# Kernel optimization log

Measured on AMD Instinct MI355X. Metric: run time of the kernel, lower is better.

The kernel has to match this reference:

```python
import jax, jax.numpy as jnp
import numpy as np

N, D_IN, D_HID, N_EXPERTS, TOP_K = 16384, 2048, 2048, 8, 2


def setup_inputs() -> dict:
    key = jax.random.key(0)
    k1, k2, k3, k4, k5 = jax.random.split(key, 5)
    x = jax.random.normal(k1, (N, D_IN), dtype=jnp.float32)
    W_experts = jax.random.normal(k2, (N_EXPERTS, D_IN, D_HID), dtype=jnp.float32) * 0.02
    b_experts = jax.random.normal(k3, (N_EXPERTS, D_HID), dtype=jnp.float32) * 0.02
    W_gate = jax.random.normal(k4, (D_IN, N_EXPERTS), dtype=jnp.float32) * 0.02
    b_gate = jax.random.normal(k5, (N_EXPERTS,), dtype=jnp.float32) * 0.02
    return {"x": x, "W_experts": W_experts, "b_experts": b_experts,
            "W_gate": W_gate, "b_gate": b_gate}


def reference(x, W_experts, b_experts, W_gate, b_gate):
    # gating softmax over experts: [N, E]
    gates = jax.nn.softmax(x @ W_gate + b_gate, axis=-1)
    # per-token top-k scores/indices: [N, K]
    top_scores, top_idx = jax.lax.top_k(gates, TOP_K)
    # FAITHFUL to original: experts chosen by the FIRST token's indices for all tokens
    idx0 = top_idx[0]                       # [K]
    W_sel = W_experts[idx0]                 # [K, D_IN, D_HID]
    b_sel = b_experts[idx0]                 # [K, D_HID]
    expert_out = jnp.einsum('ni,kio->nko', x, W_sel) + b_sel[None]  # [N, K, D_HID]
    # weight by each token's own top-k scores and sum over the K experts
    return (expert_out * top_scores[:, :, None]).sum(axis=1)        # [N, D_HID]
```

## Files before the change

kernel.cpp:

```cpp
#include <hip/hip_runtime.h>
#include <hip/hip_bf16.h>
#include <stdint.h>

#define N_TOK 16384
#define D_IN  2048
#define D_HID 2048

typedef __attribute__((ext_vector_type(8))) short  bf16x8;
typedef __attribute__((ext_vector_type(4))) float  f32x4;
typedef __attribute__((ext_vector_type(8))) unsigned short u16x8;

__device__ __forceinline__ unsigned short f2bf(float f) {
    unsigned int u = __float_as_uint(f);
    u = (u + 0x7FFFu + ((u >> 16) & 1u)) >> 16;
    return (unsigned short)u;
}

__global__ void gate_kernel(const float* __restrict__ x,
                            const float* __restrict__ Wg,
                            const float* __restrict__ bg,
                            float* __restrict__ s12,
                            int* __restrict__ eidx) {
    const int token = blockIdx.x * 4 + (threadIdx.x >> 6);
    const int lane  = threadIdx.x & 63;
    const float* xr = x + (size_t)token * D_IN;

    float acc[8];
#pragma unroll
    for (int e = 0; e < 8; ++e) acc[e] = 0.f;

    for (int i = lane; i < D_IN; i += 64) {
        float xv = xr[i];
        const float4* wr = (const float4*)(Wg + (size_t)i * 8);
        float4 w0 = wr[0], w1 = wr[1];
        acc[0] += xv * w0.x; acc[1] += xv * w0.y;
        acc[2] += xv * w0.z; acc[3] += xv * w0.w;
        acc[4] += xv * w1.x; acc[5] += xv * w1.y;
        acc[6] += xv * w1.z; acc[7] += xv * w1.w;
    }
#pragma unroll
    for (int off = 32; off > 0; off >>= 1) {
#pragma unroll
        for (int e = 0; e < 8; ++e) acc[e] += __shfl_xor(acc[e], off);
    }

    float lg[8];
    float mx = -1e30f;
#pragma unroll
    for (int e = 0; e < 8; ++e) { lg[e] = acc[e] + bg[e]; mx = fmaxf(mx, lg[e]); }
    float sum = 0.f;
#pragma unroll
    for (int e = 0; e < 8; ++e) { lg[e] = expf(lg[e] - mx); sum += lg[e]; }
    float inv = 1.f / sum;

    float s1 = -1.f, s2 = -1.f; int i1 = 0, i2 = 0;
#pragma unroll
    for (int e = 0; e < 8; ++e) {
        float g = lg[e] * inv;
        if (g > s1)      { s2 = s1; i2 = i1; s1 = g; i1 = e; }
        else if (g > s2) { s2 = g;  i2 = e; }
    }
    if (lane == 0) {
        s12[token * 2]     = s1;
        s12[token * 2 + 1] = s2;
        if (token == 0) { eidx[0] = i1; eidx[1] = i2; }
    }
}

__global__ __launch_bounds__(256) void xconv_kernel(
    const float* __restrict__ x, unsigned short* __restrict__ xb) {
    const int mt = blockIdx.x >> 6;
    const int kt = blockIdx.x & 63;
    const int t  = threadIdx.x;
    const float* src = x + ((size_t)(mt * 256 + t)) * D_IN + kt * 32;
    unsigned short* slab = xb + ((size_t)(mt * 64 + kt)) * 8192;
#pragma unroll
    for (int ks = 0; ks < 4; ++ks) {
        float4 a = *(const float4*)(src + ks * 8);
        float4 b = *(const float4*)(src + ks * 8 + 4);
        u16x8 v;
        v[0] = f2bf(a.x); v[1] = f2bf(a.y); v[2] = f2bf(a.z); v[3] = f2bf(a.w);
        v[4] = f2bf(b.x); v[5] = f2bf(b.y); v[6] = f2bf(b.z); v[7] = f2bf(b.w);
        *(u16x8*)(slab + (ks * 256 + t) * 8) = v;
    }
}

__global__ void wconv_kernel(const float* __restrict__ W,
                             const int* __restrict__ eidx,
                             unsigned short* __restrict__ wbT) {
    __shared__ float tile[64][65];
    const int be  = blockIdx.z;
    const int e   = eidx[be];
    const int k0  = blockIdx.y * 64;
    const int n0  = blockIdx.x * 64;
    const int bx  = n0 >> 7;
    const int cl0 = n0 & 127;
    const int kt0 = k0 >> 5;
    const float* src = W + (size_t)e * D_IN * D_HID;
    const int t = threadIdx.x;

#pragma unroll
    for (int p = 0; p < 4; ++p) {
        int row = p * 16 + (t >> 4);
        int col = (t & 15) * 4;
        const float* s = src + (size_t)(k0 + row) * D_HID + n0 + col;
        tile[row][col]     = s[0];
        tile[row][col + 1] = s[1];
        tile[row][col + 2] = s[2];
        tile[row][col + 3] = s[3];
    }
    __syncthreads();

    const int g   = (t >> 5) * 8;
    const int ktl = t >> 7;
    const int ks  = (t >> 5) & 3;
#pragma unroll
    for (int p = 0; p < 2; ++p) {
        int n = p * 32 + (t & 31);
        u16x8 v;
#pragma unroll
        for (int j = 0; j < 8; ++j) v[j] = f2bf(tile[g + j][n]);
        unsigned short* dst = wbT + ((size_t)(bx * 64 + kt0 + ktl)) * 8192 +
                              ((size_t)(ks * 256 + be * 128 + cl0 + n)) * 8;
        *(u16x8*)dst = v;
    }
}

#define GLD16(gp, lp)                                                        \
    __builtin_amdgcn_global_load_lds(                                        \
        (const __attribute__((address_space(1))) void*)(gp),                 \
        (__attribute__((address_space(3))) void*)(lp), 16, 0, 0)

#define LDSV(SLOT) (*(const bf16x8*)&lds[(SLOT) * 8])

#define PHASE(CB, P, T1, DOSTAGE, VMSTR)                                     \
    do {                                                                     \
        const int hb = (CB) * 4096 + ((P) >> 1) * 2048;                      \
        if (((P) & 1) == 0) {                                                \
            bC[0] = LDSV(hb + 1024 + bro);                                   \
            bC[1] = LDSV(hb + 1024 + bro + 16);                              \
            bC[2] = LDSV(hb + 1024 + bro + 32);                              \
            bC[3] = LDSV(hb + 1024 + bro + 48);                              \
        }                                                                    \
        aP[0] = LDSV(hb + aro + ((P) & 1) * 64);                             \
        aP[1] = LDSV(hb + aro + ((P) & 1) * 64 + 16);                        \
        aP[2] = LDSV(hb + aro + ((P) & 1) * 64 + 32);                        \
        aP[3] = LDSV(hb + aro + ((P) & 1) * 64 + 48);                        \
        if (DOSTAGE) {                                                       \
            const size_t so = ((size_t)(2 * (T1) + ((P) >> 1)) * 1024 +      \
                               ((P) & 1) * 512) * 8;                         \
            const int dd = ((CB) ^ 1) * 4096 + ((P) >> 1) * 2048 +           \
                           ((P) & 1) * 512 + t512;                           \
            GLD16(gA0 + so, &lds[dd * 8]);                                   \
            GLD16(gB0 + so, &lds[(dd + 1024) * 8]);                          \
        }                                                                    \
        if (VMSTR[0]) asm volatile(VMSTR ::: "memory");                      \
        __builtin_amdgcn_s_barrier();                                        \
        asm volatile("s_waitcnt lgkmcnt(0)" ::: "memory");                   \
        __builtin_amdgcn_sched_barrier(0);                                   \
        __builtin_amdgcn_s_setprio(1);                                       \
        _Pragma("unroll")                                                    \
        for (int mi = 0; mi < 4; ++mi)                                       \
            _Pragma("unroll")                                                \
            for (int ni = 0; ni < 4; ++ni)                                   \
                acc[((P) & 1) * 4 + mi][ni] =                                \
                    __builtin_amdgcn_mfma_f32_16x16x32_bf16(                 \
                        aP[mi], bC[ni], acc[((P) & 1) * 4 + mi][ni], 0, 0, 0); \
        __builtin_amdgcn_s_setprio(0);                                       \
        __builtin_amdgcn_s_barrier();                                        \
    } while (0)

__global__ __launch_bounds__(512, 2) void moe_gemm_kernel(
    const unsigned short* __restrict__ xb,
    const unsigned short* __restrict__ wbT,
    const float* __restrict__ b_exp,
    const int* __restrict__ eidx,
    const float* __restrict__ s12,
    float* __restrict__ out) {
    __shared__ __align__(16) short lds[2 * 4096 * 8];

    const int t512 = threadIdx.x;
    const int lane = t512 & 63;
    const int w    = t512 >> 6;
    const int wm   = w >> 2;
    const int wn   = w & 3;

    const int bid = blockIdx.x;
    const int xcd = bid & 7;
    const int jb  = bid >> 3;
    const int bx  = xcd * 2 + (jb & 1);
    const int by  = jb >> 1;
    const int mbase = by * 256;
    const int nbase = bx * 128;

    const unsigned short* gA0 = xb  + ((size_t)by * 64) * 8192 + t512 * 8;
    const unsigned short* gB0 = wbT + ((size_t)bx * 64) * 8192 + t512 * 8;

    const int aro = (lane >> 4) * 256 + wm * 128 + (lane & 15);
    const int bro = (lane >> 4) * 256 + wn * 64 + (lane & 15);

    f32x4 acc[8][4];
#pragma unroll
    for (int mi = 0; mi < 8; ++mi)
#pragma unroll
        for (int ni = 0; ni < 4; ++ni) acc[mi][ni] = (f32x4){0.f, 0.f, 0.f, 0.f};

    bf16x8 aP[4], bC[4];

#pragma unroll
    for (int p = 0; p < 4; ++p) {
        const size_t so = ((size_t)(p >> 1) * 1024 + (p & 1) * 512) * 8;
        const int dd = (p >> 1) * 2048 + (p & 1) * 512 + t512;
        GLD16(gA0 + so, &lds[dd * 8]);
        GLD16(gB0 + so, &lds[(dd + 1024) * 8]);
    }
    asm volatile("s_waitcnt vmcnt(4)" ::: "memory");
    __builtin_amdgcn_s_barrier();

    int cb = 0;
    for (int t = 0; t < 31; ++t) {
        PHASE(cb, 0, t + 1, 1, "");
        PHASE(cb, 1, t + 1, 1, "s_waitcnt vmcnt(4)");
        PHASE(cb, 2, t + 1, 1, "");
        PHASE(cb, 3, t + 1, 1, "s_waitcnt vmcnt(4)");
        cb ^= 1;
    }
    PHASE(1, 0, 0, 0, "");
    PHASE(1, 1, 0, 0, "s_waitcnt vmcnt(0)");
    PHASE(1, 2, 0, 0, "");
    PHASE(1, 3, 0, 0, "");

    __syncthreads();
    float* fl = (float*)lds;
    if (wn >= 2) {
        float* reg = fl + (wm * 2 + (wn - 2)) * 8192;
#pragma unroll
        for (int mi = 0; mi < 8; ++mi)
#pragma unroll
            for (int ni = 0; ni < 4; ++ni)
#pragma unroll
                for (int j = 0; j < 4; ++j) {
                    int row_l = mi * 16 + ((lane >> 4) << 2) + j;
                    int col_l = ni * 16 + (lane & 15);
                    reg[row_l * 64 + col_l] = acc[mi][ni][j];
                }
    }
    __syncthreads();
    if (wn < 2) {
        const float* reg = fl + (wm * 2 + wn) * 8192;
        const int e0 = eidx[0], e1 = eidx[1];
        const float* bb0 = b_exp + (size_t)e0 * D_HID;
        const float* bb1 = b_exp + (size_t)e1 * D_HID;
        const float2* s12v = (const float2*)s12;
        int   cc[4];
        float b0c[4], b1c[4];
#pragma unroll
        for (int ni = 0; ni < 4; ++ni) {
            cc[ni]  = nbase + wn * 64 + ni * 16 + (lane & 15);
            b0c[ni] = bb0[cc[ni]];
            b1c[ni] = bb1[cc[ni]];
        }
#pragma unroll
        for (int mi = 0; mi < 8; ++mi)
#pragma unroll
            for (int j = 0; j < 4; ++j) {
                int row_l = mi * 16 + ((lane >> 4) << 2) + j;
                int r = mbase + wm * 128 + row_l;
                float2 s = s12v[r];
#pragma unroll
                for (int ni = 0; ni < 4; ++ni) {
                    float y1 = reg[row_l * 64 + ni * 16 + (lane & 15)];
                    out[(size_t)r * D_HID + cc[ni]] =
                        s.x * (acc[mi][ni][j] + b0c[ni]) + s.y * (y1 + b1c[ni]);
                }
            }
    }
}

extern "C" void kernel_launch(void* const* d_in, const int* in_sizes, int n_in,
                              void* d_out, int out_size, void* d_ws, size_t ws_size,
                              hipStream_t stream) {
    const float* x         = (const float*)d_in[0];
    const float* W_experts = (const float*)d_in[1];
    const float* b_experts = (const float*)d_in[2];
    const float* W_gate    = (const float*)d_in[3];
    const float* b_gate    = (const float*)d_in[4];
    float* out = (float*)d_out;

    char* ws = (char*)d_ws;
    float* s12  = (float*)ws;
    int*   eidx = (int*)(ws + 131072);
    unsigned short* xb  = (unsigned short*)(ws + 262144);
    unsigned short* wbT = (unsigned short*)(ws + 262144 + 67108864);

    gate_kernel<<<N_TOK / 4, 256, 0, stream>>>(x, W_gate, b_gate, s12, eidx);
    xconv_kernel<<<4096, 256, 0, stream>>>(x, xb);
    wconv_kernel<<<dim3(32, 32, 2), 256, 0, stream>>>(W_experts, eidx, wbT);
    moe_gemm_kernel<<<1024, 512, 0, stream>>>(xb, wbT, b_experts, eidx, s12, out);
}
```

Measured before the change: 341.4 us.

## Rewrite GEMM with 32x32 MFMA, 4-stage pipeline, merge gate and x-convert kernels

The MoE GEMM now runs 256-thread blocks with 32x32x16 bf16 MFMA, so each wave computes a 128x128 sub-tile. It uses a 4-buffer LDS ring with three K tiles in flight instead of the previous double-buffered 16x16 phase scheme with barriers on both sides. The gating and x-to-bf16 conversion kernels are merged into one launch, and the gating path now handles 8 tokens per wave to reuse the W_gate loads. The intent is better MFMA density, fewer barriers and one fewer launch. In exchange the GEMM runs one block per CU with a much larger accumulator register footprint, and the new LDS addressing may create bank conflicts.

Measured after the change: 377.5 us. +10.6%, slower.

```diff
diff --git a/kernel.cpp b/kernel.cpp
--- a/kernel.cpp
+++ b/kernel.cpp
@@ -6,9 +6,9 @@
 #define D_IN  2048
 #define D_HID 2048
 
-typedef __attribute__((ext_vector_type(8))) short  bf16x8;
-typedef __attribute__((ext_vector_type(4))) float  f32x4;
-typedef __attribute__((ext_vector_type(8))) unsigned short u16x8;
+typedef __attribute__((ext_vector_type(8)))  short bf16x8;
+typedef __attribute__((ext_vector_type(16))) float f32x16;
+typedef __attribute__((ext_vector_type(8)))  unsigned short u16x8;
 
 __device__ __forceinline__ unsigned short f2bf(float f) {
     unsigned int u = __float_as_uint(f);
@@ -16,72 +16,88 @@
     return (unsigned short)u;
 }
 
-__global__ void gate_kernel(const float* __restrict__ x,
-                            const float* __restrict__ Wg,
-                            const float* __restrict__ bg,
-                            float* __restrict__ s12,
-                            int* __restrict__ eidx) {
-    const int token = blockIdx.x * 4 + (threadIdx.x >> 6);
-    const int lane  = threadIdx.x & 63;
-    const float* xr = x + (size_t)token * D_IN;
-
-    float acc[8];
-#pragma unroll
-    for (int e = 0; e < 8; ++e) acc[e] = 0.f;
+__global__ __launch_bounds__(256) void prep_kernel(
+    const float* __restrict__ x,
+    const float* __restrict__ Wg,
+    const float* __restrict__ bg,
+    unsigned short* __restrict__ xb,
+    float* __restrict__ s12,
+    int* __restrict__ eidx) {
+    const int bid = blockIdx.x;
+    if (bid < 4096) {
+        const int mt = bid >> 6;
+        const int kt = bid & 63;
+        const int t  = threadIdx.x;
+        const float* src = x + ((size_t)(mt * 256 + t)) * D_IN + kt * 32;
+        unsigned short* slab = xb + ((size_t)(mt * 64 + kt)) * 8192;
+#pragma unroll
+        for (int ks = 0; ks < 4; ++ks) {
+            float4 a = *(const float4*)(src + ks * 8);
+            float4 b = *(const float4*)(src + ks * 8 + 4);
+            u16x8 v;
+            v[0] = f2bf(a.x); v[1] = f2bf(a.y); v[2] = f2bf(a.z); v[3] = f2bf(a.w);
+            v[4] = f2bf(b.x); v[5] = f2bf(b.y); v[6] = f2bf(b.z); v[7] = f2bf(b.w);
+            *(u16x8*)(slab + (ks * 256 + t) * 8) = v;
+        }
+        return;
+    }
+    const int gb   = bid - 4096;
+    const int w    = threadIdx.x >> 6;
+    const int lane = threadIdx.x & 63;
+    const int tbase = gb * 32 + w * 8;
+
+    float acc[8][8];
+#pragma unroll
+    for (int tok = 0; tok < 8; ++tok)
+#pragma unroll
+        for (int e = 0; e < 8; ++e) acc[tok][e] = 0.f;
 
     for (int i = lane; i < D_IN; i += 64) {
-        float xv = xr[i];
         const float4* wr = (const float4*)(Wg + (size_t)i * 8);
         float4 w0 = wr[0], w1 = wr[1];
-        acc[0] += xv * w0.x; acc[1] += xv * w0.y;
-        acc[2] += xv * w0.z; acc[3] += xv * w0.w;
-        acc[4] += xv * w1.x; acc[5] += xv * w1.y;
-        acc[6] += xv * w1.z; acc[7] += xv * w1.w;
-    }
-#pragma unroll
-    for (int off = 32; off > 0; off >>= 1) {
-#pragma unroll
-        for (int e = 0; e < 8; ++e) acc[e] += __shfl_xor(acc[e], off);
-    }
-
-    float lg[8];
-    float mx = -1e30f;
-#pragma unroll
-    for (int e = 0; e < 8; ++e) { lg[e] = acc[e] + bg[e]; mx = fmaxf(mx, lg[e]); }
-    float sum = 0.f;
-#pragma unroll
-    for (int e = 0; e < 8; ++e) { lg[e] = expf(lg[e] - mx); sum += lg[e]; }
-    float inv = 1.f / sum;
-
-    float s1 = -1.f, s2 = -1.f; int i1 = 0, i2 = 0;
-#pragma unroll
-    for (int e = 0; e < 8; ++e) {
-        float g = lg[e] * inv;
-        if (g > s1)      { s2 = s1; i2 = i1; s1 = g; i1 = e; }
-        else if (g > s2) { s2 = g;  i2 = e; }
-    }
+#pragma unroll
+        for (int tok = 0; tok < 8; ++tok) {
+            float xv = x[(size_t)(tbase + tok) * D_IN + i];
+            acc[tok][0] += xv * w0.x; acc[tok][1] += xv * w0.y;
+            acc[tok][2] += xv * w0.z; acc[tok][3] += xv * w0.w;
+            acc[tok][4] += xv * w1.x; acc[tok][5] += xv * w1.y;
+            acc[tok][6] += xv * w1.z; acc[tok][7] += xv * w1.w;
+        }
+    }
+#pragma unroll
+    for (int off = 32; off > 0; off >>= 1)
+#pragma unroll
+        for (int tok = 0; tok < 8; ++tok)
+#pragma unroll
+            for (int e = 0; e < 8; ++e)
+                acc[tok][e] += __shfl_xor(acc[tok][e], off);
+
     if (lane == 0) {
-        s12[token * 2]     = s1;
-        s12[token * 2 + 1] = s2;
-        if (token == 0) { eidx[0] = i1; eidx[1] = i2; }
-    }
-}
-
-__global__ __launch_bounds__(256) void xconv_kernel(
-    const float* __restrict__ x, unsigned short* __restrict__ xb) {
-    const int mt = blockIdx.x >> 6;
-    const int kt = blockIdx.x & 63;
-    const int t  = threadIdx.x;
-    const float* src = x + ((size_t)(mt * 256 + t)) * D_IN + kt * 32;
-    unsigned short* slab = xb + ((size_t)(mt * 64 + kt)) * 8192;
-#pragma unroll
-    for (int ks = 0; ks < 4; ++ks) {
-        float4 a = *(const float4*)(src + ks * 8);
-        float4 b = *(const float4*)(src + ks * 8 + 4);
-        u16x8 v;
-        v[0] = f2bf(a.x); v[1] = f2bf(a.y); v[2] = f2bf(a.z); v[3] = f2bf(a.w);
-        v[4] = f2bf(b.x); v[5] = f2bf(b.y); v[6] = f2bf(b.z); v[7] = f2bf(b.w);
-        *(u16x8*)(slab + (ks * 256 + t) * 8) = v;
+#pragma unroll
+        for (int tok = 0; tok < 8; ++tok) {
+            float lg[8];
+            float mx = -1e30f;
+#pragma unroll
+            for (int e = 0; e < 8; ++e) {
+                lg[e] = acc[tok][e] + bg[e];
+                mx = fmaxf(mx, lg[e]);
+            }
+            float sum = 0.f;
+#pragma unroll
+            for (int e = 0; e < 8; ++e) { lg[e] = expf(lg[e] - mx); sum += lg[e]; }
+            float inv = 1.f / sum;
+            float s1 = -1.f, s2 = -1.f; int i1 = 0, i2 = 0;
+#pragma unroll
+            for (int e = 0; e < 8; ++e) {
+                float g = lg[e] * inv;
+                if (g > s1)      { s2 = s1; i2 = i1; s1 = g; i1 = e; }
+                else if (g > s2) { s2 = g;  i2 = e; }
+            }
+            const int token = tbase + tok;
+            s12[token * 2]     = s1;
+            s12[token * 2 + 1] = s2;
+            if (token == 0) { eidx[0] = i1; eidx[1] = i2; }
+        }
     }
 }
 
@@ -133,57 +149,60 @@
 
 #define LDSV(SLOT) (*(const bf16x8*)&lds[(SLOT) * 8])
 
-#define PHASE(CB, P, T1, DOSTAGE, VMSTR)                                     \
+#define STAGE(BUF, KT)                                                       \
     do {                                                                     \
-        const int hb = (CB) * 4096 + ((P) >> 1) * 2048;                      \
-        if (((P) & 1) == 0) {                                                \
-            bC[0] = LDSV(hb + 1024 + bro);                                   \
-            bC[1] = LDSV(hb + 1024 + bro + 16);                              \
-            bC[2] = LDSV(hb + 1024 + bro + 32);                              \
-            bC[3] = LDSV(hb + 1024 + bro + 48);                              \
+        _Pragma("unroll")                                                    \
+        for (int j = 0; j < 4; ++j) {                                        \
+            GLD16(gA0 + (size_t)(KT) * 8192 + j * 2048,                      \
+                  &lds[((BUF) * 2048 + j * 256 + t256) * 8]);                \
+            GLD16(gB0 + (size_t)(KT) * 8192 + j * 2048,                      \
+                  &lds[((BUF) * 2048 + 1024 + j * 256 + t256) * 8]);         \
         }                                                                    \
-        aP[0] = LDSV(hb + aro + ((P) & 1) * 64);                             \
-        aP[1] = LDSV(hb + aro + ((P) & 1) * 64 + 16);                        \
-        aP[2] = LDSV(hb + aro + ((P) & 1) * 64 + 32);                        \
-        aP[3] = LDSV(hb + aro + ((P) & 1) * 64 + 48);                        \
-        if (DOSTAGE) {                                                       \
-            const size_t so = ((size_t)(2 * (T1) + ((P) >> 1)) * 1024 +      \
-                               ((P) & 1) * 512) * 8;                         \
-            const int dd = ((CB) ^ 1) * 4096 + ((P) >> 1) * 2048 +           \
-                           ((P) & 1) * 512 + t512;                           \
-            GLD16(gA0 + so, &lds[dd * 8]);                                   \
-            GLD16(gB0 + so, &lds[(dd + 1024) * 8]);                          \
-        }                                                                    \
+    } while (0)
+
+#define TILE(BUF, STGT, DOSTAGE, VMSTR)                                      \
+    do {                                                                     \
+        __builtin_amdgcn_s_barrier();                                        \
+        if (DOSTAGE) STAGE((STGT) & 3, STGT);                                \
+        bf16x8 af[2][4], bf[2][4];                                           \
+        _Pragma("unroll")                                                    \
+        for (int kk = 0; kk < 2; ++kk)                                       \
+            _Pragma("unroll")                                                \
+            for (int q = 0; q < 4; ++q) {                                    \
+                af[kk][q] = LDSV((BUF) * 2048 + abase + kk * 512 + q * 32);  \
+                bf[kk][q] = LDSV((BUF) * 2048 + bbase + kk * 512 + q * 32);  \
+            }                                                                \
         if (VMSTR[0]) asm volatile(VMSTR ::: "memory");                      \
-        __builtin_amdgcn_s_barrier();                                        \
-        asm volatile("s_waitcnt lgkmcnt(0)" ::: "memory");                   \
-        __builtin_amdgcn_sched_barrier(0);                                   \
         __builtin_amdgcn_s_setprio(1);                                       \
         _Pragma("unroll")                                                    \
-        for (int mi = 0; mi < 4; ++mi)                                       \
+        for (int kk = 0; kk < 2; ++kk)                                       \
             _Pragma("unroll")                                                \
-            for (int ni = 0; ni < 4; ++ni)                                   \
-                acc[((P) & 1) * 4 + mi][ni] =                                \
-                    __builtin_amdgcn_mfma_f32_16x16x32_bf16(                 \
-                        aP[mi], bC[ni], acc[((P) & 1) * 4 + mi][ni], 0, 0, 0); \
+            for (int mi = 0; mi < 4; ++mi)                                   \
+                _Pragma("unroll")                                            \
+                for (int ni = 0; ni < 4; ++ni)                               \
+                    acc[mi][ni] = __builtin_amdgcn_mfma_f32_32x32x16_bf16(   \
+                        af[kk][mi], bf[kk][ni], acc[mi][ni], 0, 0, 0);       \
         __builtin_amdgcn_s_setprio(0);                                       \
-        __builtin_amdgcn_s_barrier();                                        \
     } while (0)
 
-__global__ __launch_bounds__(512, 2) void moe_gemm_kernel(
+#define VM16 "s_waitcnt vmcnt(16)"
+
+__global__ __launch_bounds__(256, 1) void moe_gemm_kernel(
     const unsigned short* __restrict__ xb,
     const unsigned short* __restrict__ wbT,
     const float* __restrict__ b_exp,
     const int* __restrict__ eidx,
     const float* __restrict__ s12,
     float* __restrict__ out) {
-    __shared__ __align__(16) short lds[2 * 4096 * 8];
-
-    const int t512 = threadIdx.x;
-    const int lane = t512 & 63;
-    const int w    = t512 >> 6;
-    const int wm   = w >> 2;
-    const int wn   = w & 3;
+    __shared__ __align__(16) short lds[8192 * 8];
+
+    const int t256 = threadIdx.x;
+    const int lane = t256 & 63;
+    const int w    = t256 >> 6;
+    const int wm   = w >> 1;
+    const int wn   = w & 1;
+    const int ls   = lane >> 5;
+    const int lr   = lane & 31;
 
     const int bid = blockIdx.x;
     const int xcd = bid & 7;
@@ -193,61 +212,53 @@
     const int mbase = by * 256;
     const int nbase = bx * 128;
 
-    const unsigned short* gA0 = xb  + ((size_t)by * 64) * 8192 + t512 * 8;
-    const unsigned short* gB0 = wbT + ((size_t)bx * 64) * 8192 + t512 * 8;
-
-    const int aro = (lane >> 4) * 256 + wm * 128 + (lane & 15);
-    const int bro = (lane >> 4) * 256 + wn * 64 + (lane & 15);
-
-    f32x4 acc[8][4];
-#pragma unroll
-    for (int mi = 0; mi < 8; ++mi)
-#pragma unroll
-        for (int ni = 0; ni < 4; ++ni) acc[mi][ni] = (f32x4){0.f, 0.f, 0.f, 0.f};
-
-    bf16x8 aP[4], bC[4];
-
-#pragma unroll
-    for (int p = 0; p < 4; ++p) {
-        const size_t so = ((size_t)(p >> 1) * 1024 + (p & 1) * 512) * 8;
-        const int dd = (p >> 1) * 2048 + (p & 1) * 512 + t512;
-        GLD16(gA0 + so, &lds[dd * 8]);
-        GLD16(gB0 + so, &lds[(dd + 1024) * 8]);
-    }
-    asm volatile("s_waitcnt vmcnt(4)" ::: "memory");
-    __builtin_amdgcn_s_barrier();
-
-    int cb = 0;
-    for (int t = 0; t < 31; ++t) {
-        PHASE(cb, 0, t + 1, 1, "");
-        PHASE(cb, 1, t + 1, 1, "s_waitcnt vmcnt(4)");
-        PHASE(cb, 2, t + 1, 1, "");
-        PHASE(cb, 3, t + 1, 1, "s_waitcnt vmcnt(4)");
-        cb ^= 1;
-    }
-    PHASE(1, 0, 0, 0, "");
-    PHASE(1, 1, 0, 0, "s_waitcnt vmcnt(0)");
-    PHASE(1, 2, 0, 0, "");
-    PHASE(1, 3, 0, 0, "");
+    const unsigned short* gA0 = xb  + ((size_t)by * 64) * 8192 + t256 * 8;
+    const unsigned short* gB0 = wbT + ((size_t)bx * 64) * 8192 + t256 * 8;
+
+    const int abase = ls * 256 + wm * 128 + lr;
+    const int bbase = 1024 + ls * 256 + wn * 128 + lr;
+
+    f32x16 acc[4][4];
+#pragma unroll
+    for (int mi = 0; mi < 4; ++mi)
+#pragma unroll
+        for (int ni = 0; ni < 4; ++ni)
+#pragma unroll
+            for (int r = 0; r < 16; ++r) acc[mi][ni][r] = 0.f;
+
+    STAGE(0, 0);
+    STAGE(1, 1);
+    STAGE(2, 2);
+    asm volatile(VM16 ::: "memory");
+
+    for (int t = 0; t < 60; t += 4) {
+        TILE(0, t + 3, 1, VM16);
+        TILE(1, t + 4, 1, VM16);
+        TILE(2, t + 5, 1, VM16);
+        TILE(3, t + 6, 1, VM16);
+    }
+    TILE(0, 63, 1, VM16);
+    TILE(1, 0, 0, "s_waitcnt vmcnt(8)");
+    TILE(2, 0, 0, "s_waitcnt vmcnt(0)");
+    TILE(3, 0, 0, "");
 
     __syncthreads();
     float* fl = (float*)lds;
-    if (wn >= 2) {
-        float* reg = fl + (wm * 2 + (wn - 2)) * 8192;
-#pragma unroll
-        for (int mi = 0; mi < 8; ++mi)
+    if (wn == 1) {
+        float* reg = fl + wm * 16384;
+#pragma unroll
+        for (int mi = 0; mi < 4; ++mi)
 #pragma unroll
             for (int ni = 0; ni < 4; ++ni)
 #pragma unroll
-                for (int j = 0; j < 4; ++j) {
-                    int row_l = mi * 16 + ((lane >> 4) << 2) + j;
-                    int col_l = ni * 16 + (lane & 15);
-                    reg[row_l * 64 + col_l] = acc[mi][ni][j];
+                for (int r = 0; r < 16; ++r) {
+                    int row_l = mi * 32 + (r & 3) + 8 * (r >> 2) + 4 * ls;
+                    reg[row_l * 128 + ni * 32 + lr] = acc[mi][ni][r];
                 }
     }
     __syncthreads();
-    if (wn < 2) {
-        const float* reg = fl + (wm * 2 + wn) * 8192;
+    if (wn == 0) {
+        const float* reg = fl + wm * 16384;
         const int e0 = eidx[0], e1 = eidx[1];
         const float* bb0 = b_exp + (size_t)e0 * D_HID;
         const float* bb1 = b_exp + (size_t)e1 * D_HID;
@@ -256,22 +267,22 @@
         float b0c[4], b1c[4];
 #pragma unroll
         for (int ni = 0; ni < 4; ++ni) {
-            cc[ni]  = nbase + wn * 64 + ni * 16 + (lane & 15);
+            cc[ni]  = nbase + ni * 32 + lr;
             b0c[ni] = bb0[cc[ni]];
             b1c[ni] = bb1[cc[ni]];
         }
 #pragma unroll
-        for (int mi = 0; mi < 8; ++mi)
-#pragma unroll
-            for (int j = 0; j < 4; ++j) {
-                int row_l = mi * 16 + ((lane >> 4) << 2) + j;
-                int r = mbase + wm * 128 + row_l;
-                float2 s = s12v[r];
+        for (int mi = 0; mi < 4; ++mi)
+#pragma unroll
+            for (int r = 0; r < 16; ++r) {
+                int row_l = mi * 32 + (r & 3) + 8 * (r >> 2) + 4 * ls;
+                int rg = mbase + wm * 128 + row_l;
+                float2 s = s12v[rg];
 #pragma unroll
                 for (int ni = 0; ni < 4; ++ni) {
-                    float y1 = reg[row_l * 64 + ni * 16 + (lane & 15)];
-                    out[(size_t)r * D_HID + cc[ni]] =
-                        s.x * (acc[mi][ni][j] + b0c[ni]) + s.y * (y1 + b1c[ni]);
+                    float y1 = reg[row_l * 128 + ni * 32 + lr];
+                    out[(size_t)rg * D_HID + cc[ni]] =
+                        s.x * (acc[mi][ni][r] + b0c[ni]) + s.y * (y1 + b1c[ni]);
                 }
             }
     }
@@ -293,8 +304,7 @@
     unsigned short* xb  = (unsigned short*)(ws + 262144);
     unsigned short* wbT = (unsigned short*)(ws + 262144 + 67108864);
 
-    gate_kernel<<<N_TOK / 4, 256, 0, stream>>>(x, W_gate, b_gate, s12, eidx);
-    xconv_kernel<<<4096, 256, 0, stream>>>(x, xb);
+    prep_kernel<<<4608, 256, 0, stream>>>(x, W_gate, b_gate, xb, s12, eidx);
     wconv_kernel<<<dim3(32, 32, 2), 256, 0, stream>>>(W_experts, eidx, wbT);
-    moe_gemm_kernel<<<1024, 512, 0, stream>>>(xb, wbT, b_experts, eidx, s12, out);
-}
+    moe_gemm_kernel<<<1024, 256, 0, stream>>>(xb, wbT, b_experts, eidx, s12, out);
+}
```
